# Kernel optimization log

Measured on AMD Instinct MI355X. Metric: run time of the kernel, lower is better.

Reference implementation:

```python
import jax, jax.numpy as jnp
import numpy as np

DIM = 384
NUM_HEADS = 12
HEAD_DIM = DIM // NUM_HEADS
SCALE = HEAD_DIM ** -0.5


def setup_inputs() -> dict:
    key = jax.random.key(0)
    k_x, k_w, k_o = jax.random.split(key, 3)
    B, n, N, C = 2, 64, 256, DIM
    x = jax.random.normal(k_x, (B, n, N, C), dtype=jnp.float32)
    # kaiming_uniform_(a=sqrt(5)) on a (3C, C) matrix -> bound = 1/sqrt(C)
    bound = 1.0 / np.sqrt(C)
    in_proj_weight = jax.random.uniform(k_w, (3 * C, C), dtype=jnp.float32, minval=-bound, maxval=bound)
    in_proj_bias = jnp.zeros((3 * C,), dtype=jnp.float32)
    ob = 1.0 / np.sqrt(C)
    out_proj_weight = jax.random.uniform(k_o, (C, C), dtype=jnp.float32, minval=-ob, maxval=ob)
    return {"x": x, "in_proj_weight": in_proj_weight, "in_proj_bias": in_proj_bias,
            "out_proj_weight": out_proj_weight}


def reference(x, in_proj_weight, in_proj_bias, out_proj_weight):
    B, n, N, C = x.shape
    H, d = NUM_HEADS, C // NUM_HEADS
    # fused QKV projection: F.linear(x, W, b) = x @ W.T + b
    qkv = jnp.einsum('bwnc,oc->bwno', x, in_proj_weight) + in_proj_bias
    q, k, v = jnp.split(qkv, 3, axis=-1)                      # each [B, n, N, C]
    # [B, n, N, C] -> [B, n, H, N, d]
    def heads(t):
        return t.reshape(B, n, N, H, d).transpose(0, 1, 3, 2, 4)
    q = heads(q) * SCALE
    k = heads(k)
    v = heads(v)
    attn = jax.nn.softmax(jnp.einsum('bwhqd,bwhkd->bwhqk', q, k), axis=-1)
    out = jnp.einsum('bwhqk,bwhkd->bwhqd', attn, v)           # [B, n, H, N, d]
    out = out.transpose(0, 1, 3, 2, 4).reshape(B, n, N, C)
    out = jnp.einsum('bwnc,oc->bwno', out, out_proj_weight)   # out_proj has no bias
    return out
```

## Files before the change

### kernel.cpp

```cpp
#include <hip/hip_runtime.h>
#include <hip/hip_bf16.h>

typedef __attribute__((ext_vector_type(4)))  float  f32x4;
typedef __attribute__((ext_vector_type(16))) float  f32x16;
typedef __attribute__((ext_vector_type(8)))  short  bf16x8;
typedef __attribute__((ext_vector_type(8)))  ushort u16x8;

#define C_DIM   384
#define QKV_DIM 1152
#define NHEAD   12
#define HDIM    32
#define NTOK    256

__device__ __forceinline__ ushort f2bf(float f) {
    union { __hip_bfloat16 h; ushort u; } cv;
    cv.h = __float2bfloat16(f);
    return cv.u;
}

__global__ void cvt_kernel(const float* __restrict__ in, ushort* __restrict__ out, int n8) {
    const int stride = gridDim.x * blockDim.x;
    for (int i = blockIdx.x * blockDim.x + threadIdx.x; i < n8; i += stride) {
        const float4 v0 = reinterpret_cast<const float4*>(in)[2 * i];
        const float4 v1 = reinterpret_cast<const float4*>(in)[2 * i + 1];
        union { ushort u[8]; u16x8 v; } o;
        o.u[0] = f2bf(v0.x); o.u[1] = f2bf(v0.y);
        o.u[2] = f2bf(v0.z); o.u[3] = f2bf(v0.w);
        o.u[4] = f2bf(v1.x); o.u[5] = f2bf(v1.y);
        o.u[6] = f2bf(v1.z); o.u[7] = f2bf(v1.w);
        reinterpret_cast<u16x8*>(out)[i] = o.v;
    }
}

template<int BIAS, int OUTF32, int AHB, int OHB>
__global__ __launch_bounds__(256, 2) void gemm_bt(const ushort* __restrict__ A,
                                                  const ushort* __restrict__ Bw,
                                                  const float* __restrict__ bias,
                                                  void* __restrict__ Cout,
                                                  int M, int N, int K) {
    __shared__ __align__(16) ushort As[2][128 * 64];
    __shared__ __align__(16) ushort Bs[2][128 * 64];

    const int t    = threadIdx.x;
    const int lane = t & 63;
    const int wave = t >> 6;
    const int wr   = (wave >> 1) * 64;
    const int wc   = (wave & 1) * 64;
    const int lr   = lane & 15;
    const int lg   = lane >> 4;

    const int gx  = gridDim.x;
    const int nwg = gx * gridDim.y;
    const int hw  = blockIdx.y * gx + blockIdx.x;
    const int cpx = nwg >> 3;
    const int lin = (hw & 7) * cpx + (hw >> 3);
    const int by  = lin / gx;
    const int bx  = lin - by * gx;
    const int mBase = by * 128;
    const int nBase = bx * 128;

    f32x4 acc[4][4] = {};
    const int nK = K >> 6;

    auto stage = [&](int kt, int c) {
        const int k0 = kt << 6;
#pragma unroll
        for (int it = 0; it < 4; ++it) {
            const int idx = it * 256 + t;
            const int r   = idx >> 3;
            const int cb  = (idx & 7) ^ (r & 7);
            const ushort* ga;
            if (AHB) {
                const int k = k0 + cb * 8;
                ga = A + ((size_t)(k >> 5) * M + (mBase + r)) * 32 + (k & 31);
            } else {
                ga = A + (size_t)(mBase + r) * K + k0 + cb * 8;
            }
            __builtin_amdgcn_global_load_lds(
                (const __attribute__((address_space(1))) void*)ga,
                (__attribute__((address_space(3))) void*)(&As[c][it * 2048 + wave * 512]),
                16, 0, 0);
        }
#pragma unroll
        for (int it = 0; it < 4; ++it) {
            const int idx = it * 256 + t;
            const int r   = idx >> 3;
            const int cb  = (idx & 7) ^ (r & 7);
            const ushort* gb = Bw + (size_t)(nBase + r) * K + k0 + cb * 8;
            __builtin_amdgcn_global_load_lds(
                (const __attribute__((address_space(1))) void*)gb,
                (__attribute__((address_space(3))) void*)(&Bs[c][it * 2048 + wave * 512]),
                16, 0, 0);
        }
    };

    stage(0, 0);
    int cur = 0;

    for (int kt = 0; kt < nK; ++kt) {
        if (kt + 1 < nK) {
            stage(kt + 1, cur ^ 1);
            asm volatile("s_waitcnt vmcnt(8)" ::: "memory");
        } else {
            asm volatile("s_waitcnt vmcnt(0)" ::: "memory");
        }
        __builtin_amdgcn_s_barrier();
        __builtin_amdgcn_sched_barrier(0);

#pragma unroll
        for (int kk = 0; kk < 2; ++kk) {
            bf16x8 af[4], bfr[4];
#pragma unroll
            for (int m = 0; m < 4; ++m) {
                const int r = wr + m * 16 + lr;
                af[m] = *reinterpret_cast<const bf16x8*>(
                    &As[cur][r * 64 + (((kk * 4 + lg) ^ (r & 7)) << 3)]);
            }
#pragma unroll
            for (int n = 0; n < 4; ++n) {
                const int r = wc + n * 16 + lr;
                bfr[n] = *reinterpret_cast<const bf16x8*>(
                    &Bs[cur][r * 64 + (((kk * 4 + lg) ^ (r & 7)) << 3)]);
            }
#pragma unroll
            for (int m = 0; m < 4; ++m)
#pragma unroll
                for (int n = 0; n < 4; ++n)
                    acc[m][n] = __builtin_amdgcn_mfma_f32_16x16x32_bf16(af[m], bfr[n], acc[m][n], 0, 0, 0);
        }

        __builtin_amdgcn_sched_barrier(0);
        __builtin_amdgcn_s_barrier();
        cur ^= 1;
    }

#pragma unroll
    for (int n = 0; n < 4; ++n) {
        const int col = nBase + wc + n * 16 + lr;
        const float bv = BIAS ? bias[col] : 0.f;
        const int sel  = OHB ? (col / 384) : 0;
        const int c384 = OHB ? (col - sel * 384) : 0;
#pragma unroll
        for (int m = 0; m < 4; ++m) {
            const int row0 = mBase + wr + m * 16 + lg * 4;
#pragma unroll
            for (int j = 0; j < 4; ++j) {
                const float v = acc[m][n][j] + bv;
                const int row = row0 + j;
                if (OUTF32) {
                    reinterpret_cast<float*>(Cout)[(size_t)row * N + col] = v;
                } else if (OHB) {
                    reinterpret_cast<ushort*>(Cout)[
                        ((size_t)(sel * NHEAD + (c384 >> 5)) * M + row) * 32 + (c384 & 31)] = f2bf(v);
                } else {
                    reinterpret_cast<ushort*>(Cout)[(size_t)row * N + col] = f2bf(v);
                }
            }
        }
    }
}

__global__ __launch_bounds__(512) void attn_kernel(const ushort* __restrict__ qkv,
                                                   ushort* __restrict__ att,
                                                   int Mtok) {
    __shared__ __align__(16) ushort Ks[NTOK * HDIM];
    __shared__ __align__(16) ushort Vt[HDIM * NTOK];

    const int bid = blockIdx.x;
    const int win = bid / NHEAD;
    const int h   = bid % NHEAD;

    const int t    = threadIdx.x;
    const int lane = t & 63;
    const int wave = t >> 6;
    const int l31  = lane & 31;
    const int h5   = lane >> 5;

    const size_t winRow = (size_t)win * NTOK;
    const ushort* Qbase = qkv + ((size_t)h * Mtok + winRow) * HDIM;
    const ushort* Kbase = qkv + ((size_t)(NHEAD + h) * Mtok + winRow) * HDIM;
    const ushort* Vbase = qkv + ((size_t)(2 * NHEAD + h) * Mtok + winRow) * HDIM;

#pragma unroll
    for (int it = 0; it < 2; ++it) {
        const int idx = it * 512 + t;
        const int key = idx >> 2;
        const int cb  = (idx & 3) ^ (key & 3);
        const ushort* gk = Kbase + key * HDIM + cb * 8;
        __builtin_amdgcn_global_load_lds(
            (const __attribute__((address_space(1))) void*)gk,
            (__attribute__((address_space(3))) void*)(&Ks[it * 4096 + wave * 512]),
            16, 0, 0);
    }
#pragma unroll
    for (int it = 0; it < 2; ++it) {
        const int idx = it * 512 + t;
        const int key = idx >> 2;
        const int cb  = idx & 3;
        u16x8 v8 = *reinterpret_cast<const u16x8*>(Vbase + key * HDIM + cb * 8);
#pragma unroll
        for (int jj = 0; jj < 8; ++jj) {
            const int dd  = cb * 8 + jj;
            const int blk = (key >> 3) ^ (dd & 7) ^ ((2 * (dd >> 3)) & 6);
            Vt[dd * NTOK + blk * 8 + (key & 7)] = v8[jj];
        }
    }
    __syncthreads();

    const float c1   = 0.25503509f;
    const int   vmsk = (l31 & 7) ^ ((2 * (l31 >> 3)) & 6);
    const int   kmsk = l31 & 3;
    const int   q0   = wave * 32;

    const int qrow = q0 + l31;
    const bf16x8 qf0 = *reinterpret_cast<const bf16x8*>(
        Qbase + (size_t)qrow * HDIM + h5 * 8);
    const bf16x8 qf1 = *reinterpret_cast<const bf16x8*>(
        Qbase + (size_t)qrow * HDIM + 16 + h5 * 8);

    float sm0 = 0.f, sm1 = 0.f, sm2 = 0.f, sm3 = 0.f;
#pragma unroll
    for (int tt = 0; tt < 8; ++tt) {
        const int key = tt * 32 + l31;
        const bf16x8 kf0 = *reinterpret_cast<const bf16x8*>(
            &Ks[key * HDIM + ((h5 ^ kmsk) << 3)]);
        const bf16x8 kf1 = *reinterpret_cast<const bf16x8*>(
            &Ks[key * HDIM + (((2 + h5) ^ kmsk) << 3)]);
        f32x16 s = {};
        s = __builtin_amdgcn_mfma_f32_32x32x16_bf16(kf0, qf0, s, 0, 0, 0);
        s = __builtin_amdgcn_mfma_f32_32x32x16_bf16(kf1, qf1, s, 0, 0, 0);
#pragma unroll
        for (int r = 0; r < 16; r += 4) {
            sm0 += __builtin_amdgcn_exp2f(s[r + 0] * c1);
            sm1 += __builtin_amdgcn_exp2f(s[r + 1] * c1);
            sm2 += __builtin_amdgcn_exp2f(s[r + 2] * c1);
            sm3 += __builtin_amdgcn_exp2f(s[r + 3] * c1);
        }
    }
    float sm = (sm0 + sm1) + (sm2 + sm3);
    sm += __shfl_xor(sm, 32, 64);
    const float inv = __builtin_amdgcn_rcpf(sm);

    f32x16 O = {};
#pragma unroll
    for (int tt = 0; tt < 8; ++tt) {
        const int key = tt * 32 + l31;
        const bf16x8 kf0 = *reinterpret_cast<const bf16x8*>(
            &Ks[key * HDIM + ((h5 ^ kmsk) << 3)]);
        const bf16x8 kf1 = *reinterpret_cast<const bf16x8*>(
            &Ks[key * HDIM + (((2 + h5) ^ kmsk) << 3)]);
        f32x16 s = {};
        s = __builtin_amdgcn_mfma_f32_32x32x16_bf16(kf0, qf0, s, 0, 0, 0);
        s = __builtin_amdgcn_mfma_f32_32x32x16_bf16(kf1, qf1, s, 0, 0, 0);

        uint pk8[8];
#pragma unroll
        for (int m = 0; m < 8; ++m) {
            const int r = 4 * (m >> 1) + 2 * (m & 1);
            const float lo = __builtin_amdgcn_exp2f(s[r + 0] * c1) * inv;
            const float hi = __builtin_amdgcn_exp2f(s[r + 1] * c1) * inv;
            uint d;
            asm("v_cvt_pk_bf16_f32 %0, %1, %2" : "=v"(d) : "v"(lo), "v"(hi));
            pk8[m] = d;
        }

#pragma unroll
        for (int k16 = 0; k16 < 2; ++k16) {
            const int mb = 4 * k16;
            const uint s0 = h5 ? pk8[mb + 0] : pk8[mb + 2];
            const uint s1 = h5 ? pk8[mb + 1] : pk8[mb + 3];
            const uint x0 = (uint)__shfl_xor((int)s0, 32, 64);
            const uint x1 = (uint)__shfl_xor((int)s1, 32, 64);
            union { uint u[4]; bf16x8 v; } pw;
            pw.u[0] = h5 ? x0 : pk8[mb + 0];
            pw.u[1] = h5 ? x1 : pk8[mb + 1];
            pw.u[2] = h5 ? pk8[mb + 2] : x0;
            pw.u[3] = h5 ? pk8[mb + 3] : x1;
            const int blk = (4 * tt + 2 * k16 + h5) ^ vmsk;
            const bf16x8 vf = *reinterpret_cast<const bf16x8*>(
                &Vt[l31 * NTOK + blk * 8]);
            O = __builtin_amdgcn_mfma_f32_32x32x16_bf16(pw.v, vf, O, 0, 0, 0);
        }
    }

    ushort* obase = att + ((size_t)h * Mtok + winRow + q0) * HDIM + l31;
#pragma unroll
    for (int r = 0; r < 16; ++r) {
        const int qr = (r & 3) + 8 * (r >> 2) + 4 * h5;
        obase[(size_t)qr * HDIM] = f2bf(O[r]);
    }
}

extern "C" void kernel_launch(void* const* d_in, const int* in_sizes, int n_in,
                              void* d_out, int out_size, void* d_ws, size_t ws_size,
                              hipStream_t stream) {
    const float* x     = (const float*)d_in[0];
    const float* w_in  = (const float*)d_in[1];
    const float* b_in  = (const float*)d_in[2];
    const float* w_out = (const float*)d_in[3];

    const int M    = in_sizes[0] / C_DIM;
    const int nWin = M / NTOK;

    char* ws = (char*)d_ws;
    size_t off = 0;
    ushort* xb    = (ushort*)(ws + off); off += (size_t)M * C_DIM * 2;
    ushort* qkvb  = (ushort*)(ws + off); off += (size_t)M * QKV_DIM * 2;
    ushort* attb  = (ushort*)(ws + off); off += (size_t)M * C_DIM * 2;
    ushort* wqkvb = (ushort*)(ws + off); off += (size_t)QKV_DIM * C_DIM * 2;
    ushort* woutb = (ushort*)(ws + off);

    cvt_kernel<<<2048, 256, 0, stream>>>(x, xb, M * C_DIM / 8);
    cvt_kernel<<<(QKV_DIM * C_DIM / 8 + 255) / 256, 256, 0, stream>>>(
        w_in, wqkvb, QKV_DIM * C_DIM / 8);
    cvt_kernel<<<(C_DIM * C_DIM / 8 + 255) / 256, 256, 0, stream>>>(
        w_out, woutb, C_DIM * C_DIM / 8);

    gemm_bt<1, 0, 0, 1><<<dim3(QKV_DIM / 128, M / 128), 256, 0, stream>>>(
        xb, wqkvb, b_in, qkvb, M, QKV_DIM, C_DIM);

    attn_kernel<<<nWin * NHEAD, 512, 0, stream>>>(qkvb, attb, M);

    gemm_bt<0, 1, 1, 0><<<dim3(C_DIM / 128, M / 128), 256, 0, stream>>>(
        attb, woutb, nullptr, d_out, M, C_DIM, C_DIM);
}
```

Before: 119.9 us.

## Process two windows per attention block with double-buffered K/V staging

Each attention block now handles two windows of the same head and prefetches the next window's K and V into a second LDS buffer while computing the current one. The aim is to hide global-load latency for K/V staging and to amortize block launch overhead. In exchange the grid shrinks by half (768 blocks instead of 1536), which may reduce parallelism across CUs. LDS use doubles to 64KB per block, which may lower occupancy.

```diff
diff --git a/kernel.cpp b/kernel.cpp
--- a/kernel.cpp
+++ b/kernel.cpp
@@ -11,6 +11,7 @@
 #define NHEAD   12
 #define HDIM    32
 #define NTOK    256
+#define WPB     2
 
 __device__ __forceinline__ ushort f2bf(float f) {
     union { __hip_bfloat16 h; ushort u; } cv;
@@ -160,15 +161,16 @@
     }
 }
 
-__global__ __launch_bounds__(512) void attn_kernel(const ushort* __restrict__ qkv,
-                                                   ushort* __restrict__ att,
-                                                   int Mtok) {
-    __shared__ __align__(16) ushort Ks[NTOK * HDIM];
-    __shared__ __align__(16) ushort Vt[HDIM * NTOK];
+__global__ __launch_bounds__(512, 4) void attn_kernel(const ushort* __restrict__ qkv,
+                                                      ushort* __restrict__ att,
+                                                      int Mtok) {
+    __shared__ __align__(16) ushort Ks[2][NTOK * HDIM];
+    __shared__ __align__(16) ushort Vt[2][NTOK * HDIM];
 
     const int bid = blockIdx.x;
-    const int win = bid / NHEAD;
     const int h   = bid % NHEAD;
+    const int wg  = bid / NHEAD;
+    const int w0  = wg * WPB;
 
     const int t    = threadIdx.x;
     const int lane = t & 63;
@@ -176,118 +178,140 @@
     const int l31  = lane & 31;
     const int h5   = lane >> 5;
 
-    const size_t winRow = (size_t)win * NTOK;
-    const ushort* Qbase = qkv + ((size_t)h * Mtok + winRow) * HDIM;
-    const ushort* Kbase = qkv + ((size_t)(NHEAD + h) * Mtok + winRow) * HDIM;
-    const ushort* Vbase = qkv + ((size_t)(2 * NHEAD + h) * Mtok + winRow) * HDIM;
-
-#pragma unroll
-    for (int it = 0; it < 2; ++it) {
-        const int idx = it * 512 + t;
-        const int key = idx >> 2;
-        const int cb  = (idx & 3) ^ (key & 3);
-        const ushort* gk = Kbase + key * HDIM + cb * 8;
-        __builtin_amdgcn_global_load_lds(
-            (const __attribute__((address_space(1))) void*)gk,
-            (__attribute__((address_space(3))) void*)(&Ks[it * 4096 + wave * 512]),
-            16, 0, 0);
-    }
-#pragma unroll
-    for (int it = 0; it < 2; ++it) {
-        const int idx = it * 512 + t;
-        const int key = idx >> 2;
-        const int cb  = idx & 3;
-        u16x8 v8 = *reinterpret_cast<const u16x8*>(Vbase + key * HDIM + cb * 8);
-#pragma unroll
-        for (int jj = 0; jj < 8; ++jj) {
-            const int dd  = cb * 8 + jj;
-            const int blk = (key >> 3) ^ (dd & 7) ^ ((2 * (dd >> 3)) & 6);
-            Vt[dd * NTOK + blk * 8 + (key & 7)] = v8[jj];
-        }
-    }
-    __syncthreads();
+    const ushort* Qh = qkv + ((size_t)h * Mtok) * HDIM;
+    const ushort* Kh = qkv + ((size_t)(NHEAD + h) * Mtok) * HDIM;
+    const ushort* Vh = qkv + ((size_t)(2 * NHEAD + h) * Mtok) * HDIM;
+
+    auto stageK = [&](int win, int c) {
+        const ushort* Kbase = Kh + (size_t)win * NTOK * HDIM;
+#pragma unroll
+        for (int it = 0; it < 2; ++it) {
+            const int idx = it * 512 + t;
+            const int key = idx >> 2;
+            const int cb  = (idx & 3) ^ (key & 3);
+            const ushort* gk = Kbase + key * HDIM + cb * 8;
+            __builtin_amdgcn_global_load_lds(
+                (const __attribute__((address_space(1))) void*)gk,
+                (__attribute__((address_space(3))) void*)(&Ks[c][it * 4096 + wave * 512]),
+                16, 0, 0);
+        }
+    };
+    auto stageV = [&](int win, int c) {
+        const ushort* Vbase = Vh + (size_t)win * NTOK * HDIM;
+#pragma unroll
+        for (int it = 0; it < 2; ++it) {
+            const int idx = it * 512 + t;
+            const int key = idx >> 2;
+            const int cbv = idx & 3;
+            u16x8 v8 = *reinterpret_cast<const u16x8*>(Vbase + key * HDIM + cbv * 8);
+#pragma unroll
+            for (int jj = 0; jj < 8; ++jj) {
+                const int dd  = cbv * 8 + jj;
+                const int blk = (key >> 3) ^ (dd & 7) ^ ((2 * (dd >> 3)) & 6);
+                Vt[c][dd * NTOK + blk * 8 + (key & 7)] = v8[jj];
+            }
+        }
+    };
 
     const float c1   = 0.25503509f;
     const int   vmsk = (l31 & 7) ^ ((2 * (l31 >> 3)) & 6);
     const int   kmsk = l31 & 3;
     const int   q0   = wave * 32;
 
-    const int qrow = q0 + l31;
-    const bf16x8 qf0 = *reinterpret_cast<const bf16x8*>(
-        Qbase + (size_t)qrow * HDIM + h5 * 8);
-    const bf16x8 qf1 = *reinterpret_cast<const bf16x8*>(
-        Qbase + (size_t)qrow * HDIM + 16 + h5 * 8);
-
-    float sm0 = 0.f, sm1 = 0.f, sm2 = 0.f, sm3 = 0.f;
-#pragma unroll
-    for (int tt = 0; tt < 8; ++tt) {
-        const int key = tt * 32 + l31;
-        const bf16x8 kf0 = *reinterpret_cast<const bf16x8*>(
-            &Ks[key * HDIM + ((h5 ^ kmsk) << 3)]);
-        const bf16x8 kf1 = *reinterpret_cast<const bf16x8*>(
-            &Ks[key * HDIM + (((2 + h5) ^ kmsk) << 3)]);
-        f32x16 s = {};
-        s = __builtin_amdgcn_mfma_f32_32x32x16_bf16(kf0, qf0, s, 0, 0, 0);
-        s = __builtin_amdgcn_mfma_f32_32x32x16_bf16(kf1, qf1, s, 0, 0, 0);
-#pragma unroll
-        for (int r = 0; r < 16; r += 4) {
-            sm0 += __builtin_amdgcn_exp2f(s[r + 0] * c1);
-            sm1 += __builtin_amdgcn_exp2f(s[r + 1] * c1);
-            sm2 += __builtin_amdgcn_exp2f(s[r + 2] * c1);
-            sm3 += __builtin_amdgcn_exp2f(s[r + 3] * c1);
-        }
-    }
-    float sm = (sm0 + sm1) + (sm2 + sm3);
-    sm += __shfl_xor(sm, 32, 64);
-    const float inv = __builtin_amdgcn_rcpf(sm);
-
-    f32x16 O = {};
-#pragma unroll
-    for (int tt = 0; tt < 8; ++tt) {
-        const int key = tt * 32 + l31;
-        const bf16x8 kf0 = *reinterpret_cast<const bf16x8*>(
-            &Ks[key * HDIM + ((h5 ^ kmsk) << 3)]);
-        const bf16x8 kf1 = *reinterpret_cast<const bf16x8*>(
-            &Ks[key * HDIM + (((2 + h5) ^ kmsk) << 3)]);
-        f32x16 s = {};
-        s = __builtin_amdgcn_mfma_f32_32x32x16_bf16(kf0, qf0, s, 0, 0, 0);
-        s = __builtin_amdgcn_mfma_f32_32x32x16_bf16(kf1, qf1, s, 0, 0, 0);
-
-        uint pk8[8];
-#pragma unroll
-        for (int m = 0; m < 8; ++m) {
-            const int r = 4 * (m >> 1) + 2 * (m & 1);
-            const float lo = __builtin_amdgcn_exp2f(s[r + 0] * c1) * inv;
-            const float hi = __builtin_amdgcn_exp2f(s[r + 1] * c1) * inv;
-            uint d;
-            asm("v_cvt_pk_bf16_f32 %0, %1, %2" : "=v"(d) : "v"(lo), "v"(hi));
-            pk8[m] = d;
-        }
-
-#pragma unroll
-        for (int k16 = 0; k16 < 2; ++k16) {
-            const int mb = 4 * k16;
-            const uint s0 = h5 ? pk8[mb + 0] : pk8[mb + 2];
-            const uint s1 = h5 ? pk8[mb + 1] : pk8[mb + 3];
-            const uint x0 = (uint)__shfl_xor((int)s0, 32, 64);
-            const uint x1 = (uint)__shfl_xor((int)s1, 32, 64);
-            union { uint u[4]; bf16x8 v; } pw;
-            pw.u[0] = h5 ? x0 : pk8[mb + 0];
-            pw.u[1] = h5 ? x1 : pk8[mb + 1];
-            pw.u[2] = h5 ? pk8[mb + 2] : x0;
-            pw.u[3] = h5 ? pk8[mb + 3] : x1;
-            const int blk = (4 * tt + 2 * k16 + h5) ^ vmsk;
-            const bf16x8 vf = *reinterpret_cast<const bf16x8*>(
-                &Vt[l31 * NTOK + blk * 8]);
-            O = __builtin_amdgcn_mfma_f32_32x32x16_bf16(pw.v, vf, O, 0, 0, 0);
-        }
-    }
-
-    ushort* obase = att + ((size_t)h * Mtok + winRow + q0) * HDIM + l31;
-#pragma unroll
-    for (int r = 0; r < 16; ++r) {
-        const int qr = (r & 3) + 8 * (r >> 2) + 4 * h5;
-        obase[(size_t)qr * HDIM] = f2bf(O[r]);
+    stageK(w0, 0); stageV(w0, 0);
+    __syncthreads();
+    int cb_ = 0;
+
+#pragma unroll 1
+    for (int i = 0; i < WPB; ++i) {
+        const int win = w0 + i;
+        if (i + 1 < WPB) { stageK(win + 1, cb_ ^ 1); stageV(win + 1, cb_ ^ 1); }
+
+        const size_t winRow = (size_t)win * NTOK;
+        const ushort* Qbase = Qh + winRow * HDIM;
+        const ushort* KsC   = Ks[cb_];
+        const ushort* VtC   = Vt[cb_];
+
+        const int qrow = q0 + l31;
+        const bf16x8 qf0 = *reinterpret_cast<const bf16x8*>(
+            Qbase + (size_t)qrow * HDIM + h5 * 8);
+        const bf16x8 qf1 = *reinterpret_cast<const bf16x8*>(
+            Qbase + (size_t)qrow * HDIM + 16 + h5 * 8);
+
+        float sm0 = 0.f, sm1 = 0.f, sm2 = 0.f, sm3 = 0.f;
+#pragma unroll
+        for (int tt = 0; tt < 8; ++tt) {
+            const int key = tt * 32 + l31;
+            const bf16x8 kf0 = *reinterpret_cast<const bf16x8*>(
+                &KsC[key * HDIM + ((h5 ^ kmsk) << 3)]);
+            const bf16x8 kf1 = *reinterpret_cast<const bf16x8*>(
+                &KsC[key * HDIM + (((2 + h5) ^ kmsk) << 3)]);
+            f32x16 s = {};
+            s = __builtin_amdgcn_mfma_f32_32x32x16_bf16(kf0, qf0, s, 0, 0, 0);
+            s = __builtin_amdgcn_mfma_f32_32x32x16_bf16(kf1, qf1, s, 0, 0, 0);
+#pragma unroll
+            for (int r = 0; r < 16; r += 4) {
+                sm0 += __builtin_amdgcn_exp2f(s[r + 0] * c1);
+                sm1 += __builtin_amdgcn_exp2f(s[r + 1] * c1);
+                sm2 += __builtin_amdgcn_exp2f(s[r + 2] * c1);
+                sm3 += __builtin_amdgcn_exp2f(s[r + 3] * c1);
+            }
+        }
+        float sm = (sm0 + sm1) + (sm2 + sm3);
+        sm += __shfl_xor(sm, 32, 64);
+        const float inv = __builtin_amdgcn_rcpf(sm);
+
+        f32x16 O = {};
+#pragma unroll
+        for (int tt = 0; tt < 8; ++tt) {
+            const int key = tt * 32 + l31;
+            const bf16x8 kf0 = *reinterpret_cast<const bf16x8*>(
+                &KsC[key * HDIM + ((h5 ^ kmsk) << 3)]);
+            const bf16x8 kf1 = *reinterpret_cast<const bf16x8*>(
+                &KsC[key * HDIM + (((2 + h5) ^ kmsk) << 3)]);
+            f32x16 s = {};
+            s = __builtin_amdgcn_mfma_f32_32x32x16_bf16(kf0, qf0, s, 0, 0, 0);
+            s = __builtin_amdgcn_mfma_f32_32x32x16_bf16(kf1, qf1, s, 0, 0, 0);
+
+            uint pk8[8];
+#pragma unroll
+            for (int m = 0; m < 8; ++m) {
+                const int r = 4 * (m >> 1) + 2 * (m & 1);
+                const float lo = __builtin_amdgcn_exp2f(s[r + 0] * c1) * inv;
+                const float hi = __builtin_amdgcn_exp2f(s[r + 1] * c1) * inv;
+                uint d;
+                asm("v_cvt_pk_bf16_f32 %0, %1, %2" : "=v"(d) : "v"(lo), "v"(hi));
+                pk8[m] = d;
+            }
+
+#pragma unroll
+            for (int k16 = 0; k16 < 2; ++k16) {
+                const int mb = 4 * k16;
+                const uint s0 = h5 ? pk8[mb + 0] : pk8[mb + 2];
+                const uint s1 = h5 ? pk8[mb + 1] : pk8[mb + 3];
+                const uint x0 = (uint)__shfl_xor((int)s0, 32, 64);
+                const uint x1 = (uint)__shfl_xor((int)s1, 32, 64);
+                union { uint u[4]; bf16x8 v; } pw;
+                pw.u[0] = h5 ? x0 : pk8[mb + 0];
+                pw.u[1] = h5 ? x1 : pk8[mb + 1];
+                pw.u[2] = h5 ? pk8[mb + 2] : x0;
+                pw.u[3] = h5 ? pk8[mb + 3] : x1;
+                const int blk = (4 * tt + 2 * k16 + h5) ^ vmsk;
+                const bf16x8 vf = *reinterpret_cast<const bf16x8*>(
+                    &VtC[l31 * NTOK + blk * 8]);
+                O = __builtin_amdgcn_mfma_f32_32x32x16_bf16(pw.v, vf, O, 0, 0, 0);
+            }
+        }
+
+        ushort* obase = att + ((size_t)h * Mtok + winRow + q0) * HDIM + l31;
+#pragma unroll
+        for (int r = 0; r < 16; ++r) {
+            const int qr = (r & 3) + 8 * (r >> 2) + 4 * h5;
+            obase[(size_t)qr * HDIM] = f2bf(O[r]);
+        }
+
+        __syncthreads();
+        cb_ ^= 1;
     }
 }
 
@@ -319,7 +343,7 @@
     gemm_bt<1, 0, 0, 1><<<dim3(QKV_DIM / 128, M / 128), 256, 0, stream>>>(
         xb, wqkvb, b_in, qkvb, M, QKV_DIM, C_DIM);
 
-    attn_kernel<<<nWin * NHEAD, 512, 0, stream>>>(qkvb, attb, M);
+    attn_kernel<<<(nWin / WPB) * NHEAD, 512, 0, stream>>>(qkvb, attb, M);
 
     gemm_bt<0, 1, 1, 0><<<dim3(C_DIM / 128, M / 128), 256, 0, stream>>>(
         attb, woutb, nullptr, d_out, M, C_DIM, C_DIM);
```

After: 253.7 us. +111.6%, slower.
